# Kernel optimization log

Measured on AMD Instinct MI355X. Metric: run time of the kernel, lower is better.

The kernel has to match this reference:

```python
import jax, jax.numpy as jnp
import numpy as np

DIM = 2048
N_HEADS = 32
N_KV_HEADS = 8
HEAD_DIM = DIM // N_HEADS  # 64
N_REP = N_HEADS // N_KV_HEADS  # 4
B, S = 2, 2048
MASK_VAL = -32768.0


def setup_inputs() -> dict:
    key = jax.random.key(0)
    ks = jax.random.split(key, 7)
    x = jax.random.normal(ks[0], (B, S, DIM), dtype=jnp.float32)
    freqs_cos = jax.random.uniform(ks[1], (S, HEAD_DIM // 2), dtype=jnp.float32)
    freqs_sin = jax.random.uniform(ks[2], (S, HEAD_DIM // 2), dtype=jnp.float32)
    sc = 1.0 / np.sqrt(DIM)
    wq = jax.random.normal(ks[3], (N_HEADS * HEAD_DIM, DIM), dtype=jnp.float32) * sc
    wk = jax.random.normal(ks[4], (N_KV_HEADS * HEAD_DIM, DIM), dtype=jnp.float32) * sc
    wv = jax.random.normal(ks[5], (N_KV_HEADS * HEAD_DIM, DIM), dtype=jnp.float32) * sc
    wo = jax.random.normal(ks[6], (DIM, N_HEADS * HEAD_DIM), dtype=jnp.float32) * sc
    return {"x": x, "freqs_cos": freqs_cos, "freqs_sin": freqs_sin,
            "wq": wq, "wk": wk, "wv": wv, "wo": wo}


def _apply_rope(q, k, cos, sin):
    # q: [B,S,H,D], k: [B,S,Hkv,D]; interleaved real/imag pairs in last dim
    def rot(t):
        tr = t.reshape(t.shape[:-1] + (-1, 2))  # [..., D/2, 2]
        t_r, t_i = tr[..., 0], tr[..., 1]
        c = cos[None, :, None, :]  # broadcast over batch and heads
        s = sin[None, :, None, :]
        o_r = t_r * c - t_i * s
        o_i = t_r * s + t_i * c
        return jnp.stack([o_r, o_i], axis=-1).reshape(t.shape)
    return rot(q), rot(k)


def reference(x, freqs_cos, freqs_sin, wq, wk, wv, wo):
    bsz, seqlen, _ = x.shape
    xq = (x @ wq.T).reshape(bsz, seqlen, N_HEADS, HEAD_DIM)
    xk = (x @ wk.T).reshape(bsz, seqlen, N_KV_HEADS, HEAD_DIM)
    xv = (x @ wv.T).reshape(bsz, seqlen, N_KV_HEADS, HEAD_DIM)
    xq, xk = _apply_rope(xq, xk, freqs_cos, freqs_sin)
    # GQA: repeat each kv head n_rep times contiguously (matches per-head cat loop)
    xk = jnp.repeat(xk, N_REP, axis=2)  # [B,S,H,D]
    xv = jnp.repeat(xv, N_REP, axis=2)
    # [B,H,S,D]
    q = xq.transpose(0, 2, 1, 3)
    k = xk.transpose(0, 2, 1, 3)
    v = xv.transpose(0, 2, 1, 3)
    scores = jnp.einsum('bhqd,bhkd->bhqk', q, k) / jnp.sqrt(jnp.float32(HEAD_DIM))
    causal = jnp.triu(jnp.full((seqlen, seqlen), MASK_VAL, dtype=scores.dtype), k=1)
    scores = scores + causal[None, None, :, :]
    probs = jax.nn.softmax(scores.astype(jnp.float32), axis=-1).astype(q.dtype)
    out = jnp.einsum('bhqk,bhkd->bhqd', probs, v)
    out = out.transpose(0, 2, 1, 3).reshape(bsz, seqlen, -1)
    return out @ wo.T
```

## Files before the change

### kernel.cpp

```cpp
#include <hip/hip_runtime.h>
#include <hip/hip_bf16.h>
#include <type_traits>

typedef __bf16 bf16;
typedef __bf16 bf16x2 __attribute__((ext_vector_type(2)));
typedef __bf16 bf16x4 __attribute__((ext_vector_type(4)));
typedef __bf16 bf16x8 __attribute__((ext_vector_type(8)));
typedef float f32x4 __attribute__((ext_vector_type(4)));

#define AS1 __attribute__((address_space(1)))
#define AS3 __attribute__((address_space(3)))

#define KAPPA 0.180336880111f

__device__ __forceinline__ void load_lds16(const void* g, void* l) {
  __builtin_amdgcn_global_load_lds((AS1 void*)g, (AS3 void*)l, 16, 0, 0);
}
__device__ __forceinline__ float exp2_fast(float x) {
  return __builtin_amdgcn_exp2f(x);
}

__global__ void f2b_all(const float* __restrict__ x, const float* __restrict__ wq,
                        const float* __restrict__ wk, const float* __restrict__ wv,
                        const float* __restrict__ wo, bf16* __restrict__ xb,
                        bf16* __restrict__ wqkv, bf16* __restrict__ wob) {
  int bid = blockIdx.x;
  const float* src;
  bf16* dst;
  int off;
  if (bid < 8192) { src = x; dst = xb; off = bid; }
  else if (bid < 12288) { src = wq; dst = wqkv; off = bid - 8192; }
  else if (bid < 13312) { src = wk; dst = wqkv + 4194304; off = bid - 12288; }
  else if (bid < 14336) { src = wv; dst = wqkv + 5242880; off = bid - 13312; }
  else { src = wo; dst = wob; off = bid - 14336; }
  int i = (off * 256 + threadIdx.x) * 4;
  float4 v = *(const float4*)(src + i);
  bf16x4 o = {(bf16)v.x, (bf16)v.y, (bf16)v.z, (bf16)v.w};
  *(bf16x4*)(dst + i) = o;
}

__global__ __launch_bounds__(256, 3) void gemm_qkv(const bf16* __restrict__ A,
                                                   const bf16* __restrict__ Bw,
                                                   const float* __restrict__ fc,
                                                   const float* __restrict__ fs,
                                                   bf16* __restrict__ Qro,
                                                   bf16* __restrict__ Kro,
                                                   bf16* __restrict__ Vt) {
  const int K = 2048;
  __shared__ bf16 As[3][128][32];
  __shared__ bf16 Bs[3][128][32];
  const int t = threadIdx.x;
  const int wave = t >> 6, lane = t & 63, qd = lane >> 4, ln = lane & 15;
  const int wm = (wave >> 1) * 64;
  const int wn = (wave & 1) * 64;
  const int bn = blockIdx.x;
  const size_t bm = (size_t)blockIdx.y * 128;

  const bf16* Ab = A + bm * (size_t)K;
  const bf16* Bb = Bw + (size_t)bn * 128 * K;

  auto stage = [&](const bf16* gb, char* lb, int tk, int slot) {
#pragma unroll
    for (int sub = 0; sub < 2; sub++) {
      int e = sub * 256 + t;
      int ro = e >> 2, gs = (e & 3) ^ ((ro >> 1) & 3);
      load_lds16(gb + (size_t)ro * K + tk * 32 + gs * 8,
                 lb + slot * 8192 + sub * 4096 + wave * 1024);
    }
  };

  stage(Ab, (char*)As, 0, 0);
  stage(Bb, (char*)Bs, 0, 0);
  stage(Ab, (char*)As, 1, 1);
  stage(Bb, (char*)Bs, 1, 1);
  asm volatile("s_waitcnt vmcnt(4)" ::: "memory");
  __builtin_amdgcn_s_barrier();

  f32x4 acc[4][4] = {};
  const int segoff = (qd ^ ((ln >> 1) & 3)) << 4;

  int cs = 0, ps = 2;
  for (int tk = 0; tk < 64; tk++) {
    if (tk < 62) {
      stage(Ab, (char*)As, tk + 2, ps);
      stage(Bb, (char*)Bs, tk + 2, ps);
    }
    const char* Asl = (const char*)As + cs * 8192;
    const char* Bsl = (const char*)Bs + cs * 8192;

    bf16x8 af[4], bfr[4];
#pragma unroll
    for (int i = 0; i < 4; i++)
      af[i] = *(const bf16x8*)(Asl + (wm + i * 16 + ln) * 64 + segoff);
#pragma unroll
    for (int j = 0; j < 4; j++)
      bfr[j] = *(const bf16x8*)(Bsl + (wn + j * 16 + ln) * 64 + segoff);

    asm volatile("s_waitcnt lgkmcnt(0)" ::: "memory");
    __builtin_amdgcn_sched_barrier(0);
    __builtin_amdgcn_s_setprio(1);
#pragma unroll
    for (int i = 0; i < 4; i++)
#pragma unroll
      for (int j = 0; j < 4; j++)
        acc[i][j] = __builtin_amdgcn_mfma_f32_16x16x32_bf16(af[i], bfr[j],
                                                            acc[i][j], 0, 0, 0);
    __builtin_amdgcn_s_setprio(0);

    if (tk < 62) asm volatile("s_waitcnt vmcnt(4)" ::: "memory");
    else if (tk == 62) asm volatile("s_waitcnt vmcnt(0)" ::: "memory");
    __builtin_amdgcn_s_barrier();
    cs = (cs == 2) ? 0 : cs + 1;
    ps = (ps == 2) ? 0 : ps + 1;
  }

  const int b = (int)(bm >> 11);
  const int sb = (int)(bm & 2047) + wm;
  const bool odd = ln & 1;

  if (bn < 20) {
    const bool isQ = bn < 16;
    const float kap = isQ ? KAPPA : 1.0f;
    const int hh = isQ ? (bn * 2 + (wn >> 6)) : ((bn - 16) * 2 + (wn >> 6));
    bf16* dst = isQ ? (Qro + ((size_t)(b * 32 + hh) * 2048) * 64)
                    : (Kro + ((size_t)(b * 8 + hh) * 2048) * 64);
#pragma unroll
    for (int i = 0; i < 4; i++) {
#pragma unroll
      for (int j = 0; j < 4; j++) {
        const int d = j * 16 + ln;
        const int i_f = d >> 1;
#pragma unroll
        for (int r = 0; r < 4; r++) {
          int s = sb + i * 16 + qd * 4 + r;
          float v = acc[i][j][r];
          float p = __shfl_xor(v, 1);
          float cv = fc[s * 32 + i_f] * kap;
          float sv = fs[s * 32 + i_f] * kap;
          float o = odd ? (p * sv + v * cv) : (v * cv - p * sv);
          dst[(size_t)s * 64 + d] = (bf16)o;
        }
      }
    }
  } else {
    const int kh = (bn - 20) * 2 + (wn >> 6);
#pragma unroll
    for (int i = 0; i < 4; i++)
#pragma unroll
      for (int j = 0; j < 4; j++) {
        const int d = j * 16 + ln;
        int s = sb + i * 16 + qd * 4;
        bf16x4 ov = {(bf16)acc[i][j][0], (bf16)acc[i][j][1],
                     (bf16)acc[i][j][2], (bf16)acc[i][j][3]};
        *(bf16x4*)&Vt[((size_t)(b * 8 + kh) * 64 + d) * 2048 + s] = ov;
      }
  }
}

__global__ __launch_bounds__(256, 2) void gemm_bt(const bf16* __restrict__ A,
                                                  const bf16* __restrict__ Bw,
                                                  float* __restrict__ C) {
  const int K = 2048, N = 2048;
  __shared__ bf16 As[3][128][32];
  __shared__ bf16 Bs[3][128][32];
  const int t = threadIdx.x;
  const int wave = t >> 6, lane = t & 63, qd = lane >> 4, ln = lane & 15;
  const int wm = (wave >> 1) * 64;
  const int wn = (wave & 1) * 64;
  const size_t bm = (size_t)blockIdx.y * 128;
  const size_t bn = (size_t)blockIdx.x * 128;

  const bf16* Ab = A + bm * (size_t)K;
  const bf16* Bb = Bw + bn * (size_t)K;

  auto stage = [&](const bf16* gb, char* lb, int tk, int slot) {
#pragma unroll
    for (int sub = 0; sub < 2; sub++) {
      int e = sub * 256 + t;
      int ro = e >> 2, gs = (e & 3) ^ ((ro >> 1) & 3);
      load_lds16(gb + (size_t)ro * K + tk * 32 + gs * 8,
                 lb + slot * 8192 + sub * 4096 + wave * 1024);
    }
  };

  stage(Ab, (char*)As, 0, 0);
  stage(Bb, (char*)Bs, 0, 0);
  stage(Ab, (char*)As, 1, 1);
  stage(Bb, (char*)Bs, 1, 1);
  asm volatile("s_waitcnt vmcnt(4)" ::: "memory");
  __builtin_amdgcn_s_barrier();

  f32x4 acc[4][4] = {};
  const int segoff = (qd ^ ((ln >> 1) & 3)) << 4;

  int cs = 0, ps = 2;
  for (int tk = 0; tk < 64; tk++) {
    if (tk < 62) {
      stage(Ab, (char*)As, tk + 2, ps);
      stage(Bb, (char*)Bs, tk + 2, ps);
    }
    const char* Asl = (const char*)As + cs * 8192;
    const char* Bsl = (const char*)Bs + cs * 8192;

    bf16x8 af[4], bfr[4];
#pragma unroll
    for (int i = 0; i < 4; i++)
      af[i] = *(const bf16x8*)(Asl + (wm + i * 16 + ln) * 64 + segoff);
#pragma unroll
    for (int j = 0; j < 4; j++)
      bfr[j] = *(const bf16x8*)(Bsl + (wn + j * 16 + ln) * 64 + segoff);

    asm volatile("s_waitcnt lgkmcnt(0)" ::: "memory");
    __builtin_amdgcn_sched_barrier(0);
    __builtin_amdgcn_s_setprio(1);
#pragma unroll
    for (int i = 0; i < 4; i++)
#pragma unroll
      for (int j = 0; j < 4; j++)
        acc[i][j] = __builtin_amdgcn_mfma_f32_16x16x32_bf16(af[i], bfr[j],
                                                            acc[i][j], 0, 0, 0);
    __builtin_amdgcn_s_setprio(0);

    if (tk < 62) asm volatile("s_waitcnt vmcnt(4)" ::: "memory");
    else if (tk == 62) asm volatile("s_waitcnt vmcnt(0)" ::: "memory");
    __builtin_amdgcn_s_barrier();
    cs = (cs == 2) ? 0 : cs + 1;
    ps = (ps == 2) ? 0 : ps + 1;
  }

#pragma unroll
  for (int i = 0; i < 4; i++)
#pragma unroll
    for (int j = 0; j < 4; j++)
#pragma unroll
      for (int r = 0; r < 4; r++) {
        size_t row = bm + wm + i * 16 + qd * 4 + r;
        size_t col = bn + wn + j * 16 + ln;
        C[row * N + col] = acc[i][j][r];
      }
}

__global__ __launch_bounds__(256, 3) void attn_fwd(const bf16* __restrict__ Q,
                                                   const bf16* __restrict__ Kg,
                                                   const bf16* __restrict__ Vg,
                                                   bf16* __restrict__ O) {
  __shared__ bf16 Ks[2][64][64];
  __shared__ bf16 Vs[2][64][64];
  __shared__ bf16 Ps[128][64];
  const int t = threadIdx.x;
  const int wave = t >> 6, lane = t & 63, qd = lane >> 4, ln = lane & 15;
  const int bid = blockIdx.x;
  const int qt = 15 - (bid >> 6);
  const int bh = bid & 63;
  const int b = bh >> 5, h = bh & 31, kh = h >> 2;
  const bf16* Qb = Q + ((size_t)(b * 32 + h) * 2048 + qt * 128) * 64;
  const bf16* Kb = Kg + (size_t)(b * 8 + kh) * 2048 * 64;
  const bf16* Vb = Vg + (size_t)(b * 8 + kh) * 64 * 2048;
  char* PsB = (char*)Ps;

  bf16x8 qf[2][2];
#pragma unroll
  for (int kk = 0; kk < 2; kk++)
#pragma unroll
    for (int mi = 0; mi < 2; mi++)
      qf[kk][mi] = *(const bf16x8*)(Qb + (wave * 32 + mi * 16 + ln) * 64 +
                                    (kk * 4 + qd) * 8);

  auto stageKV = [&](int kb, int buf) {
#pragma unroll
    for (int i = 0; i < 2; i++) {
      int e = i * 256 + t;
      int row = e >> 3, sg = (e & 7) ^ (row & 7);
      load_lds16(Kb + (size_t)(kb * 64 + row) * 64 + sg * 8,
                 (char*)Ks + buf * 8192 + i * 4096 + wave * 1024);
      load_lds16(Vb + (size_t)row * 2048 + kb * 64 + sg * 8,
                 (char*)Vs + buf * 8192 + i * 4096 + wave * 1024);
    }
  };

  f32x4 o_acc[4][2] = {};
  float l_st[2] = {0.f, 0.f};
  const int q0 = qt * 128 + wave * 32;
  const int nkb = 2 * qt + 2;

  stageKV(0, 0);
  __syncthreads();

  for (int kb = 0; kb < nkb; kb++) {
    const int cur = kb & 1;
    if (kb + 1 < nkb) stageKV(kb + 1, cur ^ 1);
    const char* Ksl = (const char*)Ks + cur * 8192;
    const char* Vsl = (const char*)Vs + cur * 8192;

    f32x4 s_acc[4][2] = {};
#pragma unroll
    for (int kk = 0; kk < 2; kk++) {
      bf16x8 ak[4];
#pragma unroll
      for (int j = 0; j < 4; j++) {
        int row = j * 16 + ln;
        int ph = (kk * 4 + qd) ^ (ln & 7);
        ak[j] = *(const bf16x8*)(Ksl + row * 128 + ph * 16);
      }
#pragma unroll
      for (int j = 0; j < 4; j++)
#pragma unroll
        for (int mi = 0; mi < 2; mi++)
          s_acc[j][mi] = __builtin_amdgcn_mfma_f32_16x16x32_bf16(
              ak[j], qf[kk][mi], s_acc[j][mi], 0, 0, 0);
    }

    auto smax = [&](auto maskc) {
      constexpr bool MASK = decltype(maskc)::value;
#pragma unroll
      for (int mi = 0; mi < 2; mi++) {
        const int qv = q0 + mi * 16 + ln;
        const int prow = wave * 32 + mi * 16 + ln;
        float rs = 0.f;
#pragma unroll
        for (int j = 0; j < 4; j++) {
          bf16x4 pk;
#pragma unroll
          for (int r = 0; r < 4; r++) {
            float s = s_acc[j][mi][r];
            if (MASK) {
              int k_glob = kb * 64 + j * 16 + qd * 4 + r;
              if (k_glob > qv) s = -1e5f;
            }
            float pv = exp2_fast(s - 16.f);
            rs += pv;
            pk[r] = (bf16)pv;
          }
          int ps = (j * 2 + (qd >> 1)) ^ (ln & 7);
          *(bf16x4*)(PsB + prow * 128 + ps * 16 + (qd & 1) * 8) = pk;
        }
        l_st[mi] += rs;
      }
    };
    if (kb * 64 + 63 > q0) smax(std::true_type{});
    else smax(std::false_type{});

#pragma unroll
    for (int kk = 0; kk < 2; kk++) {
      bf16x8 av[4], bp[2];
#pragma unroll
      for (int dj = 0; dj < 4; dj++) {
        int row = dj * 16 + ln;
        int ph = (kk * 4 + qd) ^ (ln & 7);
        av[dj] = *(const bf16x8*)(Vsl + row * 128 + ph * 16);
      }
#pragma unroll
      for (int mi = 0; mi < 2; mi++) {
        int prow = wave * 32 + mi * 16 + ln;
        int ph = (kk * 4 + qd) ^ (ln & 7);
        bp[mi] = *(const bf16x8*)(PsB + prow * 128 + ph * 16);
      }
#pragma unroll
      for (int dj = 0; dj < 4; dj++)
#pragma unroll
        for (int mi = 0; mi < 2; mi++)
          o_acc[dj][mi] = __builtin_amdgcn_mfma_f32_16x16x32_bf16(
              av[dj], bp[mi], o_acc[dj][mi], 0, 0, 0);
    }

    __syncthreads();
  }

#pragma unroll
  for (int mi = 0; mi < 2; mi++) {
    float lt = l_st[mi];
    lt += __shfl_xor(lt, 16);
    lt += __shfl_xor(lt, 32);
    float inv = 1.f / lt;
    int q_idx = qt * 128 + wave * 32 + mi * 16 + ln;
#pragma unroll
    for (int dj = 0; dj < 4; dj++) {
      bf16x4 ov;
#pragma unroll
      for (int r = 0; r < 4; r++) ov[r] = (bf16)(o_acc[dj][mi][r] * inv);
      *(bf16x4*)&O[((size_t)(b * 2048 + q_idx) * 32 + h) * 64 + dj * 16 + qd * 4] = ov;
    }
  }
}

extern "C" void kernel_launch(void* const* d_in, const int* in_sizes, int n_in,
                              void* d_out, int out_size, void* d_ws,
                              size_t ws_size, hipStream_t stream) {
  const float* x = (const float*)d_in[0];
  const float* fc = (const float*)d_in[1];
  const float* fs = (const float*)d_in[2];
  const float* wq = (const float*)d_in[3];
  const float* wk = (const float*)d_in[4];
  const float* wv = (const float*)d_in[5];
  const float* wo = (const float*)d_in[6];
  float* out = (float*)d_out;

  char* ws = (char*)d_ws;
  const size_t MB = (size_t)1 << 20;
  bf16* xb   = (bf16*)(ws + 0 * MB);
  bf16* wqkv = (bf16*)(ws + 16 * MB);
  bf16* wob  = (bf16*)(ws + 28 * MB);
  bf16* Qro  = (bf16*)(ws + 36 * MB);
  bf16* Kro  = (bf16*)(ws + 52 * MB);
  bf16* Vt   = (bf16*)(ws + 56 * MB);
  bf16* Oa   = (bf16*)(ws + 60 * MB);

  dim3 blk(256);
  f2b_all<<<18432, blk, 0, stream>>>(x, wq, wk, wv, wo, xb, wqkv, wob);
  gemm_qkv<<<dim3(24, 32), blk, 0, stream>>>(xb, wqkv, fc, fs, Qro, Kro, Vt);
  attn_fwd<<<1024, blk, 0, stream>>>(Qro, Kro, Vt, Oa);
  gemm_bt<<<dim3(16, 32), blk, 0, stream>>>(Oa, wob, out);
}
```

Baseline: 282.3 us.

## Double-buffer GEMM register fragments and prefetch LDS reads one step ahead

Both bf16 GEMM kernels (QKV projection with RoPE epilogue, and output projection) now read the next k-step's A/B fragments from LDS into a second register set while the MFMAs of the current step run. Global-to-LDS staging now runs three tiles ahead, with a matching prologue and adjusted vmcnt waits. The loop is manually unrolled by two to swap the fragment buffers. This aims to hide LDS read latency behind MFMA work, at the cost of more VGPRs and tighter buffer-reuse ordering across three LDS slots.

```diff
diff --git a/kernel.cpp b/kernel.cpp
--- a/kernel.cpp
+++ b/kernel.cpp
@@ -69,49 +69,62 @@
     }
   };
 
+  f32x4 acc[4][4] = {};
+  const int segoff = (qd ^ ((ln >> 1) & 3)) << 4;
+  bf16x8 fa0[4], fb0[4], fa1[4], fb1[4];
+
   stage(Ab, (char*)As, 0, 0);
   stage(Bb, (char*)Bs, 0, 0);
   stage(Ab, (char*)As, 1, 1);
   stage(Bb, (char*)Bs, 1, 1);
-  asm volatile("s_waitcnt vmcnt(4)" ::: "memory");
+  stage(Ab, (char*)As, 2, 2);
+  stage(Bb, (char*)Bs, 2, 2);
+  asm volatile("s_waitcnt vmcnt(8)" ::: "memory");
   __builtin_amdgcn_s_barrier();
-
-  f32x4 acc[4][4] = {};
-  const int segoff = (qd ^ ((ln >> 1) & 3)) << 4;
-
-  int cs = 0, ps = 2;
-  for (int tk = 0; tk < 64; tk++) {
-    if (tk < 62) {
-      stage(Ab, (char*)As, tk + 2, ps);
-      stage(Bb, (char*)Bs, tk + 2, ps);
-    }
-    const char* Asl = (const char*)As + cs * 8192;
-    const char* Bsl = (const char*)Bs + cs * 8192;
-
-    bf16x8 af[4], bfr[4];
+#pragma unroll
+  for (int i = 0; i < 4; i++) {
+    fa0[i] = *(const bf16x8*)((const char*)As + (wm + i * 16 + ln) * 64 + segoff);
+    fb0[i] = *(const bf16x8*)((const char*)Bs + (wn + i * 16 + ln) * 64 + segoff);
+  }
+  asm volatile("s_waitcnt lgkmcnt(0) vmcnt(4)" ::: "memory");
+  __builtin_amdgcn_sched_barrier(0);
+  __builtin_amdgcn_s_barrier();
+
+  auto step = [&](int tk, bf16x8 (&ca)[4], bf16x8 (&cb)[4],
+                  bf16x8 (&na)[4], bf16x8 (&nb)[4]) {
+    if (tk < 61) {
+      stage(Ab, (char*)As, tk + 3, tk % 3);
+      stage(Bb, (char*)Bs, tk + 3, tk % 3);
+    }
+    if (tk < 63) {
+      const char* Asl = (const char*)As + ((tk + 1) % 3) * 8192;
+      const char* Bsl = (const char*)Bs + ((tk + 1) % 3) * 8192;
+#pragma unroll
+      for (int i = 0; i < 4; i++) {
+        na[i] = *(const bf16x8*)(Asl + (wm + i * 16 + ln) * 64 + segoff);
+        nb[i] = *(const bf16x8*)(Bsl + (wn + i * 16 + ln) * 64 + segoff);
+      }
+    }
+    __builtin_amdgcn_s_setprio(1);
 #pragma unroll
     for (int i = 0; i < 4; i++)
-      af[i] = *(const bf16x8*)(Asl + (wm + i * 16 + ln) * 64 + segoff);
-#pragma unroll
-    for (int j = 0; j < 4; j++)
-      bfr[j] = *(const bf16x8*)(Bsl + (wn + j * 16 + ln) * 64 + segoff);
-
-    asm volatile("s_waitcnt lgkmcnt(0)" ::: "memory");
-    __builtin_amdgcn_sched_barrier(0);
-    __builtin_amdgcn_s_setprio(1);
-#pragma unroll
-    for (int i = 0; i < 4; i++)
 #pragma unroll
       for (int j = 0; j < 4; j++)
-        acc[i][j] = __builtin_amdgcn_mfma_f32_16x16x32_bf16(af[i], bfr[j],
+        acc[i][j] = __builtin_amdgcn_mfma_f32_16x16x32_bf16(ca[i], cb[j],
                                                             acc[i][j], 0, 0, 0);
     __builtin_amdgcn_s_setprio(0);
-
-    if (tk < 62) asm volatile("s_waitcnt vmcnt(4)" ::: "memory");
-    else if (tk == 62) asm volatile("s_waitcnt vmcnt(0)" ::: "memory");
-    __builtin_amdgcn_s_barrier();
-    cs = (cs == 2) ? 0 : cs + 1;
-    ps = (ps == 2) ? 0 : ps + 1;
+    if (tk < 63) {
+      if (tk < 61) asm volatile("s_waitcnt lgkmcnt(0) vmcnt(4)" ::: "memory");
+      else if (tk == 61) asm volatile("s_waitcnt lgkmcnt(0) vmcnt(0)" ::: "memory");
+      else asm volatile("s_waitcnt lgkmcnt(0)" ::: "memory");
+      __builtin_amdgcn_sched_barrier(0);
+      __builtin_amdgcn_s_barrier();
+    }
+  };
+
+  for (int tk = 0; tk < 64; tk += 2) {
+    step(tk, fa0, fb0, fa1, fb1);
+    step(tk + 1, fa1, fb1, fa0, fb0);
   }
 
   const int b = (int)(bm >> 11);
@@ -183,49 +196,62 @@
     }
   };
 
+  f32x4 acc[4][4] = {};
+  const int segoff = (qd ^ ((ln >> 1) & 3)) << 4;
+  bf16x8 fa0[4], fb0[4], fa1[4], fb1[4];
+
   stage(Ab, (char*)As, 0, 0);
   stage(Bb, (char*)Bs, 0, 0);
   stage(Ab, (char*)As, 1, 1);
   stage(Bb, (char*)Bs, 1, 1);
-  asm volatile("s_waitcnt vmcnt(4)" ::: "memory");
+  stage(Ab, (char*)As, 2, 2);
+  stage(Bb, (char*)Bs, 2, 2);
+  asm volatile("s_waitcnt vmcnt(8)" ::: "memory");
   __builtin_amdgcn_s_barrier();
-
-  f32x4 acc[4][4] = {};
-  const int segoff = (qd ^ ((ln >> 1) & 3)) << 4;
-
-  int cs = 0, ps = 2;
-  for (int tk = 0; tk < 64; tk++) {
-    if (tk < 62) {
-      stage(Ab, (char*)As, tk + 2, ps);
-      stage(Bb, (char*)Bs, tk + 2, ps);
-    }
-    const char* Asl = (const char*)As + cs * 8192;
-    const char* Bsl = (const char*)Bs + cs * 8192;
-
-    bf16x8 af[4], bfr[4];
+#pragma unroll
+  for (int i = 0; i < 4; i++) {
+    fa0[i] = *(const bf16x8*)((const char*)As + (wm + i * 16 + ln) * 64 + segoff);
+    fb0[i] = *(const bf16x8*)((const char*)Bs + (wn + i * 16 + ln) * 64 + segoff);
+  }
+  asm volatile("s_waitcnt lgkmcnt(0) vmcnt(4)" ::: "memory");
+  __builtin_amdgcn_sched_barrier(0);
+  __builtin_amdgcn_s_barrier();
+
+  auto step = [&](int tk, bf16x8 (&ca)[4], bf16x8 (&cb)[4],
+                  bf16x8 (&na)[4], bf16x8 (&nb)[4]) {
+    if (tk < 61) {
+      stage(Ab, (char*)As, tk + 3, tk % 3);
+      stage(Bb, (char*)Bs, tk + 3, tk % 3);
+    }
+    if (tk < 63) {
+      const char* Asl = (const char*)As + ((tk + 1) % 3) * 8192;
+      const char* Bsl = (const char*)Bs + ((tk + 1) % 3) * 8192;
+#pragma unroll
+      for (int i = 0; i < 4; i++) {
+        na[i] = *(const bf16x8*)(Asl + (wm + i * 16 + ln) * 64 + segoff);
+        nb[i] = *(const bf16x8*)(Bsl + (wn + i * 16 + ln) * 64 + segoff);
+      }
+    }
+    __builtin_amdgcn_s_setprio(1);
 #pragma unroll
     for (int i = 0; i < 4; i++)
-      af[i] = *(const bf16x8*)(Asl + (wm + i * 16 + ln) * 64 + segoff);
-#pragma unroll
-    for (int j = 0; j < 4; j++)
-      bfr[j] = *(const bf16x8*)(Bsl + (wn + j * 16 + ln) * 64 + segoff);
-
-    asm volatile("s_waitcnt lgkmcnt(0)" ::: "memory");
-    __builtin_amdgcn_sched_barrier(0);
-    __builtin_amdgcn_s_setprio(1);
-#pragma unroll
-    for (int i = 0; i < 4; i++)
 #pragma unroll
       for (int j = 0; j < 4; j++)
-        acc[i][j] = __builtin_amdgcn_mfma_f32_16x16x32_bf16(af[i], bfr[j],
+        acc[i][j] = __builtin_amdgcn_mfma_f32_16x16x32_bf16(ca[i], cb[j],
                                                             acc[i][j], 0, 0, 0);
     __builtin_amdgcn_s_setprio(0);
-
-    if (tk < 62) asm volatile("s_waitcnt vmcnt(4)" ::: "memory");
-    else if (tk == 62) asm volatile("s_waitcnt vmcnt(0)" ::: "memory");
-    __builtin_amdgcn_s_barrier();
-    cs = (cs == 2) ? 0 : cs + 1;
-    ps = (ps == 2) ? 0 : ps + 1;
+    if (tk < 63) {
+      if (tk < 61) asm volatile("s_waitcnt lgkmcnt(0) vmcnt(4)" ::: "memory");
+      else if (tk == 61) asm volatile("s_waitcnt lgkmcnt(0) vmcnt(0)" ::: "memory");
+      else asm volatile("s_waitcnt lgkmcnt(0)" ::: "memory");
+      __builtin_amdgcn_sched_barrier(0);
+      __builtin_amdgcn_s_barrier();
+    }
+  };
+
+  for (int tk = 0; tk < 64; tk += 2) {
+    step(tk, fa0, fb0, fa1, fb1);
+    step(tk + 1, fa1, fb1, fa0, fb0);
   }
 
 #pragma unroll
```

Result: faster. 276.0 us (-2.2%).

## Pre-swizzle weights into MFMA fragment layout and load B directly to registers

Applied to the files above, without the earlier changes.

The weight conversion kernel now writes wq/wk/wv/wo in a tiled layout matching the MFMA B-fragment order, so each lane reads its 16-byte operand straight from global memory. Both GEMMs drop the B shared-memory buffers and instead double-buffer B fragments in registers, prefetched one k-step ahead, while A stays in a 3-stage LDS pipeline. This removes half the LDS traffic and LDS footprint, which may allow more occupancy. The cost is more register pressure and per-wave global loads of B that are not shared through LDS across waves.

```diff
diff --git a/kernel.cpp b/kernel.cpp
--- a/kernel.cpp
+++ b/kernel.cpp
@@ -25,18 +25,30 @@
                         const float* __restrict__ wo, bf16* __restrict__ xb,
                         bf16* __restrict__ wqkv, bf16* __restrict__ wob) {
   int bid = blockIdx.x;
+  if (bid < 8192) {
+    int i = (bid * 256 + threadIdx.x) * 4;
+    float4 v = *(const float4*)(x + i);
+    bf16x4 o = {(bf16)v.x, (bf16)v.y, (bf16)v.z, (bf16)v.w};
+    *(bf16x4*)(xb + i) = o;
+    return;
+  }
   const float* src;
   bf16* dst;
   int off;
-  if (bid < 8192) { src = x; dst = xb; off = bid; }
-  else if (bid < 12288) { src = wq; dst = wqkv; off = bid - 8192; }
-  else if (bid < 13312) { src = wk; dst = wqkv + 4194304; off = bid - 12288; }
-  else if (bid < 14336) { src = wv; dst = wqkv + 5242880; off = bid - 13312; }
-  else { src = wo; dst = wob; off = bid - 14336; }
-  int i = (off * 256 + threadIdx.x) * 4;
-  float4 v = *(const float4*)(src + i);
-  bf16x4 o = {(bf16)v.x, (bf16)v.y, (bf16)v.z, (bf16)v.w};
-  *(bf16x4*)(dst + i) = o;
+  if (bid < 10240) { src = wq; dst = wqkv; off = bid - 8192; }
+  else if (bid < 10752) { src = wk; dst = wqkv + 4194304; off = bid - 10240; }
+  else if (bid < 11264) { src = wv; dst = wqkv + 5242880; off = bid - 10752; }
+  else { src = wo; dst = wob; off = bid - 11264; }
+  int i = (off * 256 + threadIdx.x) * 8;
+  int n = i >> 11, k = i & 2047;
+  float4 v0 = *(const float4*)(src + (size_t)n * 2048 + k);
+  float4 v1 = *(const float4*)(src + (size_t)n * 2048 + k + 4);
+  bf16x8 o = {(bf16)v0.x, (bf16)v0.y, (bf16)v0.z, (bf16)v0.w,
+              (bf16)v1.x, (bf16)v1.y, (bf16)v1.z, (bf16)v1.w};
+  size_t dstb = ((size_t)((n >> 6) * 64 + (k >> 5))) * 4096 +
+                (size_t)((n >> 4) & 3) * 1024 +
+                (size_t)((n & 15) | (((k >> 3) & 3) << 4)) * 16;
+  *(bf16x8*)((char*)dst + dstb) = o;
 }
 
 __global__ __launch_bounds__(256, 3) void gemm_qkv(const bf16* __restrict__ A,
@@ -48,7 +60,6 @@
                                                    bf16* __restrict__ Vt) {
   const int K = 2048;
   __shared__ bf16 As[3][128][32];
-  __shared__ bf16 Bs[3][128][32];
   const int t = threadIdx.x;
   const int wave = t >> 6, lane = t & 63, qd = lane >> 4, ln = lane & 15;
   const int wm = (wave >> 1) * 64;
@@ -57,61 +68,61 @@
   const size_t bm = (size_t)blockIdx.y * 128;
 
   const bf16* Ab = A + bm * (size_t)K;
-  const bf16* Bb = Bw + (size_t)bn * 128 * K;
-
-  auto stage = [&](const bf16* gb, char* lb, int tk, int slot) {
+  const int n0 = bn * 2 + (wn >> 6);
+  const char* Bb = (const char*)Bw + (size_t)n0 * 262144 + (size_t)lane * 16;
+
+  auto stage = [&](int tk, int slot) {
 #pragma unroll
     for (int sub = 0; sub < 2; sub++) {
       int e = sub * 256 + t;
       int ro = e >> 2, gs = (e & 3) ^ ((ro >> 1) & 3);
-      load_lds16(gb + (size_t)ro * K + tk * 32 + gs * 8,
-                 lb + slot * 8192 + sub * 4096 + wave * 1024);
+      load_lds16(Ab + (size_t)ro * K + tk * 32 + gs * 8,
+                 (char*)As + slot * 8192 + sub * 4096 + wave * 1024);
     }
   };
-
-  stage(Ab, (char*)As, 0, 0);
-  stage(Bb, (char*)Bs, 0, 0);
-  stage(Ab, (char*)As, 1, 1);
-  stage(Bb, (char*)Bs, 1, 1);
-  asm volatile("s_waitcnt vmcnt(4)" ::: "memory");
-  __builtin_amdgcn_s_barrier();
 
   f32x4 acc[4][4] = {};
   const int segoff = (qd ^ ((ln >> 1) & 3)) << 4;
-
-  int cs = 0, ps = 2;
-  for (int tk = 0; tk < 64; tk++) {
-    if (tk < 62) {
-      stage(Ab, (char*)As, tk + 2, ps);
-      stage(Bb, (char*)Bs, tk + 2, ps);
-    }
-    const char* Asl = (const char*)As + cs * 8192;
-    const char* Bsl = (const char*)Bs + cs * 8192;
-
-    bf16x8 af[4], bfr[4];
+  bf16x8 b0[4], b1[4];
+
+#pragma unroll
+  for (int j = 0; j < 4; j++)
+    b0[j] = *(const bf16x8*)(Bb + (size_t)j * 1024);
+  stage(0, 0);
+  stage(1, 1);
+  asm volatile("s_waitcnt vmcnt(2)" ::: "memory");
+  __builtin_amdgcn_s_barrier();
+
+  auto step = [&](int tk, bf16x8 (&cb)[4], bf16x8 (&nb)[4]) {
+    if (tk < 62) stage(tk + 2, (tk + 2) % 3);
+    if (tk < 63) {
+#pragma unroll
+      for (int j = 0; j < 4; j++)
+        nb[j] = *(const bf16x8*)(Bb + (size_t)(tk + 1) * 4096 + j * 1024);
+    }
+    const char* Asl = (const char*)As + (tk % 3) * 8192;
+    bf16x8 af[4];
 #pragma unroll
     for (int i = 0; i < 4; i++)
       af[i] = *(const bf16x8*)(Asl + (wm + i * 16 + ln) * 64 + segoff);
-#pragma unroll
-    for (int j = 0; j < 4; j++)
-      bfr[j] = *(const bf16x8*)(Bsl + (wn + j * 16 + ln) * 64 + segoff);
-
-    asm volatile("s_waitcnt lgkmcnt(0)" ::: "memory");
+    if (tk <= 61) asm volatile("s_waitcnt lgkmcnt(0) vmcnt(6)" ::: "memory");
+    else if (tk == 62) asm volatile("s_waitcnt lgkmcnt(0) vmcnt(4)" ::: "memory");
+    else asm volatile("s_waitcnt lgkmcnt(0) vmcnt(0)" ::: "memory");
     __builtin_amdgcn_sched_barrier(0);
     __builtin_amdgcn_s_setprio(1);
 #pragma unroll
     for (int i = 0; i < 4; i++)
 #pragma unroll
       for (int j = 0; j < 4; j++)
-        acc[i][j] = __builtin_amdgcn_mfma_f32_16x16x32_bf16(af[i], bfr[j],
+        acc[i][j] = __builtin_amdgcn_mfma_f32_16x16x32_bf16(af[i], cb[j],
                                                             acc[i][j], 0, 0, 0);
     __builtin_amdgcn_s_setprio(0);
-
-    if (tk < 62) asm volatile("s_waitcnt vmcnt(4)" ::: "memory");
-    else if (tk == 62) asm volatile("s_waitcnt vmcnt(0)" ::: "memory");
-    __builtin_amdgcn_s_barrier();
-    cs = (cs == 2) ? 0 : cs + 1;
-    ps = (ps == 2) ? 0 : ps + 1;
+    if (tk < 63) __builtin_amdgcn_s_barrier();
+  };
+
+  for (int tk = 0; tk < 64; tk += 2) {
+    step(tk, b0, b1);
+    step(tk + 1, b1, b0);
   }
 
   const int b = (int)(bm >> 11);
@@ -162,7 +173,6 @@
                                                   float* __restrict__ C) {
   const int K = 2048, N = 2048;
   __shared__ bf16 As[3][128][32];
-  __shared__ bf16 Bs[3][128][32];
   const int t = threadIdx.x;
   const int wave = t >> 6, lane = t & 63, qd = lane >> 4, ln = lane & 15;
   const int wm = (wave >> 1) * 64;
@@ -171,61 +181,61 @@
   const size_t bn = (size_t)blockIdx.x * 128;
 
   const bf16* Ab = A + bm * (size_t)K;
-  const bf16* Bb = Bw + bn * (size_t)K;
-
-  auto stage = [&](const bf16* gb, char* lb, int tk, int slot) {
+  const int n0 = (int)(bn >> 6) + (wn >> 6);
+  const char* Bb = (const char*)Bw + (size_t)n0 * 262144 + (size_t)lane * 16;
+
+  auto stage = [&](int tk, int slot) {
 #pragma unroll
     for (int sub = 0; sub < 2; sub++) {
       int e = sub * 256 + t;
       int ro = e >> 2, gs = (e & 3) ^ ((ro >> 1) & 3);
-      load_lds16(gb + (size_t)ro * K + tk * 32 + gs * 8,
-                 lb + slot * 8192 + sub * 4096 + wave * 1024);
+      load_lds16(Ab + (size_t)ro * K + tk * 32 + gs * 8,
+                 (char*)As + slot * 8192 + sub * 4096 + wave * 1024);
     }
   };
-
-  stage(Ab, (char*)As, 0, 0);
-  stage(Bb, (char*)Bs, 0, 0);
-  stage(Ab, (char*)As, 1, 1);
-  stage(Bb, (char*)Bs, 1, 1);
-  asm volatile("s_waitcnt vmcnt(4)" ::: "memory");
-  __builtin_amdgcn_s_barrier();
 
   f32x4 acc[4][4] = {};
   const int segoff = (qd ^ ((ln >> 1) & 3)) << 4;
-
-  int cs = 0, ps = 2;
-  for (int tk = 0; tk < 64; tk++) {
-    if (tk < 62) {
-      stage(Ab, (char*)As, tk + 2, ps);
-      stage(Bb, (char*)Bs, tk + 2, ps);
-    }
-    const char* Asl = (const char*)As + cs * 8192;
-    const char* Bsl = (const char*)Bs + cs * 8192;
-
-    bf16x8 af[4], bfr[4];
+  bf16x8 b0[4], b1[4];
+
+#pragma unroll
+  for (int j = 0; j < 4; j++)
+    b0[j] = *(const bf16x8*)(Bb + (size_t)j * 1024);
+  stage(0, 0);
+  stage(1, 1);
+  asm volatile("s_waitcnt vmcnt(2)" ::: "memory");
+  __builtin_amdgcn_s_barrier();
+
+  auto step = [&](int tk, bf16x8 (&cb)[4], bf16x8 (&nb)[4]) {
+    if (tk < 62) stage(tk + 2, (tk + 2) % 3);
+    if (tk < 63) {
+#pragma unroll
+      for (int j = 0; j < 4; j++)
+        nb[j] = *(const bf16x8*)(Bb + (size_t)(tk + 1) * 4096 + j * 1024);
+    }
+    const char* Asl = (const char*)As + (tk % 3) * 8192;
+    bf16x8 af[4];
 #pragma unroll
     for (int i = 0; i < 4; i++)
       af[i] = *(const bf16x8*)(Asl + (wm + i * 16 + ln) * 64 + segoff);
-#pragma unroll
-    for (int j = 0; j < 4; j++)
-      bfr[j] = *(const bf16x8*)(Bsl + (wn + j * 16 + ln) * 64 + segoff);
-
-    asm volatile("s_waitcnt lgkmcnt(0)" ::: "memory");
+    if (tk <= 61) asm volatile("s_waitcnt lgkmcnt(0) vmcnt(6)" ::: "memory");
+    else if (tk == 62) asm volatile("s_waitcnt lgkmcnt(0) vmcnt(4)" ::: "memory");
+    else asm volatile("s_waitcnt lgkmcnt(0) vmcnt(0)" ::: "memory");
     __builtin_amdgcn_sched_barrier(0);
     __builtin_amdgcn_s_setprio(1);
 #pragma unroll
     for (int i = 0; i < 4; i++)
 #pragma unroll
       for (int j = 0; j < 4; j++)
-        acc[i][j] = __builtin_amdgcn_mfma_f32_16x16x32_bf16(af[i], bfr[j],
+        acc[i][j] = __builtin_amdgcn_mfma_f32_16x16x32_bf16(af[i], cb[j],
                                                             acc[i][j], 0, 0, 0);
     __builtin_amdgcn_s_setprio(0);
-
-    if (tk < 62) asm volatile("s_waitcnt vmcnt(4)" ::: "memory");
-    else if (tk == 62) asm volatile("s_waitcnt vmcnt(0)" ::: "memory");
-    __builtin_amdgcn_s_barrier();
-    cs = (cs == 2) ? 0 : cs + 1;
-    ps = (ps == 2) ? 0 : ps + 1;
+    if (tk < 63) __builtin_amdgcn_s_barrier();
+  };
+
+  for (int tk = 0; tk < 64; tk += 2) {
+    step(tk, b0, b1);
+    step(tk + 1, b1, b0);
   }
 
 #pragma unroll
@@ -406,7 +416,7 @@
   bf16* Oa   = (bf16*)(ws + 60 * MB);
 
   dim3 blk(256);
-  f2b_all<<<18432, blk, 0, stream>>>(x, wq, wk, wv, wo, xb, wqkv, wob);
+  f2b_all<<<13312, blk, 0, stream>>>(x, wq, wk, wv, wo, xb, wqkv, wob);
   gemm_qkv<<<dim3(24, 32), blk, 0, stream>>>(xb, wqkv, fc, fs, Qro, Kro, Vt);
   attn_fwd<<<1024, blk, 0, stream>>>(Qro, Kro, Vt, Oa);
   gemm_bt<<<dim3(16, 32), blk, 0, stream>>>(Oa, wob, out);
```

Result: slower. 291.2 us (+3.2%).
